# Kernel tuning notes

Hardware: AMD Instinct MI355X
Metric: run time of the kernel (lower is better)

## Reference

```python
import jax, jax.numpy as jnp
import numpy as np

N_NODES = 50000
N_EDGES = 800000
IN_C, HID_C, OUT_C = 256, 256, 128


def gcn_conv(x, W, b, row, col, n_nodes):
    """PyG GCNConv: linear transform, symmetric-normalized aggregation, bias.
    row/col already include self-loops. Messages flow row -> col."""
    h = x @ W  # [N, out]
    deg = jax.ops.segment_sum(jnp.ones_like(col, dtype=h.dtype), col, num_segments=n_nodes)
    d_inv_sqrt = jnp.where(deg > 0, jax.lax.rsqrt(jnp.maximum(deg, 1e-12)), 0.0)
    norm = d_inv_sqrt[row] * d_inv_sqrt[col]  # [E]
    msg = h[row] * norm[:, None]              # gather + scale, [E, out]
    out = jax.ops.segment_sum(msg, col, num_segments=n_nodes)  # scatter-add
    return out + b


def setup_inputs() -> dict:
    key = jax.random.key(0)
    k_x, k_e, k_w1, k_w2 = jax.random.split(key, 4)
    x = jax.random.normal(k_x, (N_NODES, IN_C), dtype=jnp.float32)
    edge_index = jax.random.randint(k_e, (2, N_EDGES), 0, N_NODES, dtype=jnp.int64)
    # Glorot-style init for GCN weights, zeros bias (PyG default)
    s1 = float(np.sqrt(6.0 / (IN_C + HID_C)))
    s2 = float(np.sqrt(6.0 / (HID_C + OUT_C)))
    W1 = jax.random.uniform(k_w1, (IN_C, HID_C), dtype=jnp.float32, minval=-s1, maxval=s1)
    b1 = jnp.zeros((HID_C,), dtype=jnp.float32)
    W2 = jax.random.uniform(k_w2, (HID_C, OUT_C), dtype=jnp.float32, minval=-s2, maxval=s2)
    b2 = jnp.zeros((OUT_C,), dtype=jnp.float32)
    return {"x": x, "edge_index": edge_index, "W1": W1, "b1": b1, "W2": W2, "b2": b2}


def reference(x, edge_index, W1, b1, W2, b2):
    n = x.shape[0]
    # add self-loops (PyG GCNConv default add_self_loops=True)
    loops = jnp.arange(n, dtype=edge_index.dtype)
    row = jnp.concatenate([edge_index[0], loops])
    col = jnp.concatenate([edge_index[1], loops])
    h = gcn_conv(x, W1, b1, row, col, n)
    h = jax.nn.relu(h)  # dropout p=0.0 -> identity
    out = gcn_conv(h, W2, b2, row, col, n)
    return out
```

## Files before the change

### kernel.cpp

```cpp
#include <hip/hip_runtime.h>

#define NN 50000
#define NE 800000
#define IN_C 256
#define HID_C 256
#define OUT_C 128

#define NETP (NE + 8 * NN)
#define NBUCK 196
#define CHUNK 4096
#define NPA 196
#define CAP_B 6400

typedef unsigned short u16;
typedef unsigned int u32;
typedef __attribute__((ext_vector_type(8))) short short8;
typedef __attribute__((ext_vector_type(8))) unsigned short ushort8;
typedef __attribute__((ext_vector_type(4))) float f32x4;
typedef __attribute__((ext_vector_type(2))) float f32x2;
typedef __attribute__((ext_vector_type(4))) unsigned u32x4;

#define CPS ((size_t)(NN + 1) * 32)

__device__ __forceinline__ u16 f2b(float f) {
  unsigned int u = __float_as_uint(f);
  return (u16)((u + 0x7FFFu + ((u >> 16) & 1u)) >> 16);
}
__device__ __forceinline__ float b2f(u16 s) {
  return __uint_as_float(((unsigned int)s) << 16);
}


__global__ __launch_bounds__(256) void convw_zero(const float* __restrict__ W1,
                                                  const float* __restrict__ W2,
                                                  u16* __restrict__ W1t,
                                                  u16* __restrict__ W2t,
                                                  int* __restrict__ cnt,
                                                  u16* __restrict__ Hb,
                                                  int nzb) {
  int b = blockIdx.x;
  if (b < 256) {
    int id = b * 256 + threadIdx.x;
    if (id < 256 * 256) {
      int n = id >> 8, k = id & 255;
      W1t[id] = f2b(W1[k * 256 + n]);
    }
    if (id < 128 * 256) {
      int n = id >> 8, k = id & 255;
      W2t[id] = f2b(W2[k * 128 + n]);
    }
  } else if (b < 256 + nzb) {
    int i = (b - 256) * 256 + threadIdx.x;
    if (i < NN) cnt[i] = 1;
  } else {
    int t = threadIdx.x;
    Hb[(size_t)(t >> 5) * CPS + (size_t)NN * 32 + (t & 31)] = 0;
  }
}


__global__ __launch_bounds__(256) void hist_kernel(const int* __restrict__ col,
                                                   int* __restrict__ cnt, int E) {
  int e = blockIdx.x * blockDim.x + threadIdx.x;
  if (e < E) atomicAdd(&cnt[col[e]], 1);
}

__global__ __launch_bounds__(256) void passA_hist(const int* __restrict__ col,
                                                  int* __restrict__ cntmat, int E) {
  __shared__ int hcnt[256];
  const int blk = blockIdx.x;
  const int tid = threadIdx.x;
  hcnt[tid] = 0;
  __syncthreads();
  const int e0 = blk * CHUNK;
#pragma unroll
  for (int j = 0; j < 16; ++j) {
    int e = e0 + j * 256 + tid;
    if (e < E) atomicAdd(&hcnt[col[e] >> 8], 1);
  }
  __syncthreads();
  cntmat[tid * 256 + blk] = hcnt[tid];
}

__global__ __launch_bounds__(256) void passA_scan(const int* __restrict__ cntmat,
                                                  const int* __restrict__ row_off,
                                                  int* __restrict__ gbase,
                                                  int* __restrict__ btot) {
  __shared__ int wsum[4], wpre[4];
  const int b = blockIdx.x;
  const int tid = threadIdx.x;
  int lane = tid & 63, wid = tid >> 6;
  int v = (tid < NPA) ? cntmat[b * 256 + tid] : 0;
  int s = v;
#pragma unroll
  for (int off = 1; off < 64; off <<= 1) {
    int t = __shfl_up(s, off, 64);
    if (lane >= off) s += t;
  }
  if (lane == 63) wsum[wid] = s;
  __syncthreads();
  if (tid == 0) {
    int acc = 0;
#pragma unroll
    for (int w = 0; w < 4; ++w) { wpre[w] = acc; acc += wsum[w]; }
  }
  __syncthreads();
  int bstart = row_off[b << 8];
  gbase[b * 256 + tid] = bstart + wpre[wid] + (s - v);
  if (tid == 255) btot[b] = wpre[3] + s;
}

__global__ __launch_bounds__(256) void scan1_kernel(const int* __restrict__ cnt,
                                                    int* __restrict__ bsum, int n) {
  __shared__ int ws[4];
  int i = blockIdx.x * 256 + threadIdx.x;
  int lane = threadIdx.x & 63, wid = threadIdx.x >> 6;
  int v = (i < n) ? ((cnt[i] + 7) & ~7) : 0;
#pragma unroll
  for (int off = 32; off > 0; off >>= 1) v += __shfl_down(v, off, 64);
  if (lane == 0) ws[wid] = v;
  __syncthreads();
  if (threadIdx.x == 0) bsum[blockIdx.x] = ws[0] + ws[1] + ws[2] + ws[3];
}

__global__ __launch_bounds__(256) void scan2_kernel(const int* __restrict__ bsum,
                                                    int* __restrict__ boff,
                                                    int* __restrict__ row_off,
                                                    int nb, int n) {
  __shared__ int wsum[4], wpre[5];
  int lane = threadIdx.x & 63, wid = threadIdx.x >> 6;
  int v = (threadIdx.x < nb) ? bsum[threadIdx.x] : 0;
  int s = v;
#pragma unroll
  for (int off = 1; off < 64; off <<= 1) {
    int t = __shfl_up(s, off, 64);
    if (lane >= off) s += t;
  }
  if (lane == 63) wsum[wid] = s;
  __syncthreads();
  if (threadIdx.x == 0) {
    int acc = 0;
#pragma unroll
    for (int w = 0; w < 4; ++w) { wpre[w] = acc; acc += wsum[w]; }
    wpre[4] = acc;
  }
  __syncthreads();
  if (threadIdx.x < nb) boff[threadIdx.x] = wpre[wid] + (s - v);
  if (threadIdx.x == 0) row_off[n] = wpre[4];
}

__global__ __launch_bounds__(256) void scan3_kernel(const int* __restrict__ cnt,
                                                    const int* __restrict__ boff,
                                                    int* __restrict__ row_off,
                                                    float* __restrict__ dinv, int n) {
  __shared__ int wsum[4], wpre[4];
  int i = blockIdx.x * 256 + threadIdx.x;
  int lane = threadIdx.x & 63, wid = threadIdx.x >> 6;
  int vr = (i < n) ? cnt[i] : 0;
  int v = (vr + 7) & ~7;
  int s = v;
#pragma unroll
  for (int off = 1; off < 64; off <<= 1) {
    int t = __shfl_up(s, off, 64);
    if (lane >= off) s += t;
  }
  if (lane == 63) wsum[wid] = s;
  __syncthreads();
  if (threadIdx.x == 0) {
    int acc = 0;
#pragma unroll
    for (int w = 0; w < 4; ++w) { wpre[w] = acc; acc += wsum[w]; }
  }
  __syncthreads();
  if (i < n) {
    int off = boff[blockIdx.x] + wpre[wid] + (s - v);
    row_off[i] = off;
    dinv[i] = rsqrtf((float)vr);
  }
}


template <bool A_IS_F32, bool PLANAR_C>
__device__ __forceinline__ void gemm_body(const void* __restrict__ Ap,
                                          const u16* __restrict__ Bt,
                                          const float* __restrict__ dscale,
                                          u16* __restrict__ C, int M, int N,
                                          int bx, int by,
                                          u16 (&Asl)[2][5120], u16 (&Bsl)[2][5120]) {
  const int tid = threadIdx.x;
  const int row0 = by * 128;
  const int col0 = bx * 128;

  f32x4 acc[4][4] = {};

  const int seg = tid & 7;
  const int rb = tid >> 3;
  const int wave = tid >> 6, lane = tid & 63;
  const int wm = wave >> 1, wn = wave & 1;
  const int qr = lane & 15, quad = lane >> 4;

  float4 aF[4];
  ushort4 aU[4];
  ushort4 bR[4];

  auto load_tiles = [&](int k0) {
    if constexpr (A_IS_F32) {
      const float* A = (const float*)Ap;
#pragma unroll
      for (int i = 0; i < 4; ++i) {
        int gr = row0 + rb + i * 32;
        aF[i] = (gr < M) ? *(const float4*)&A[(size_t)gr * 256 + k0 + seg * 4]
                         : make_float4(0.f, 0.f, 0.f, 0.f);
      }
    } else {
      const u16* A = (const u16*)Ap;
#pragma unroll
      for (int i = 0; i < 4; ++i) {
        int gr = row0 + rb + i * 32;
        aU[i] = (gr < M) ? *(const ushort4*)&A[(size_t)gr * 256 + k0 + seg * 4]
                         : make_ushort4(0, 0, 0, 0);
      }
    }
#pragma unroll
    for (int i = 0; i < 4; ++i) {
      int n = rb + i * 32;
      bR[i] = *(const ushort4*)&Bt[(size_t)(col0 + n) * 256 + k0 + seg * 4];
    }
  };

  auto write_lds = [&](int buf) {
#pragma unroll
    for (int i = 0; i < 4; ++i) {
      int r = rb + i * 32;
      ushort4 u;
      if constexpr (A_IS_F32) {
        u.x = f2b(aF[i].x); u.y = f2b(aF[i].y);
        u.z = f2b(aF[i].z); u.w = f2b(aF[i].w);
      } else {
        u = aU[i];
      }
      *(ushort4*)&Asl[buf][r * 40 + seg * 4] = u;
      *(ushort4*)&Bsl[buf][r * 40 + seg * 4] = bR[i];
    }
  };

  load_tiles(0);
  write_lds(0);
  __syncthreads();

#pragma unroll
  for (int it = 0; it < 8; ++it) {
    const int cur = it & 1;
    if (it < 7) load_tiles((it + 1) * 32);

    short8 afr[4], bfr[4];
#pragma unroll
    for (int mt = 0; mt < 4; ++mt)
      afr[mt] = *(const short8*)&Asl[cur][(wm * 64 + mt * 16 + qr) * 40 + quad * 8];
#pragma unroll
    for (int nt = 0; nt < 4; ++nt)
      bfr[nt] = *(const short8*)&Bsl[cur][(wn * 64 + nt * 16 + qr) * 40 + quad * 8];
#pragma unroll
    for (int mt = 0; mt < 4; ++mt)
#pragma unroll
      for (int nt = 0; nt < 4; ++nt)
        acc[mt][nt] = __builtin_amdgcn_mfma_f32_16x16x32_bf16(afr[mt], bfr[nt], acc[mt][nt], 0, 0, 0);

    if (it < 7) {
      write_lds(1 - cur);
      __syncthreads();
    }
  }

#pragma unroll
  for (int mt = 0; mt < 4; ++mt) {
#pragma unroll
    for (int i = 0; i < 4; ++i) {
      int gr = row0 + wm * 64 + mt * 16 + quad * 4 + i;
      if (gr < M) {
        float sc = dscale[gr];
#pragma unroll
        for (int nt = 0; nt < 4; ++nt) {
          int gc = col0 + wn * 64 + nt * 16 + qr;
          u16 val = f2b(acc[mt][nt][i] * sc);
          if constexpr (PLANAR_C)
            C[(size_t)(gc >> 5) * CPS + (size_t)gr * 32 + (gc & 31)] = val;
          else
            C[(size_t)gr * N + gc] = val;
        }
      }
    }
  }
}

template <bool A_IS_F32, bool PLANAR_C>
__global__ __launch_bounds__(256) void gemm_mfma(const void* __restrict__ Ap,
                                                 const u16* __restrict__ Bt,
                                                 const float* __restrict__ dscale,
                                                 u16* __restrict__ C, int M, int N,
                                                 u16* __restrict__ zrow) {
  if (zrow != nullptr && blockIdx.x == 0 && blockIdx.y == 0 && threadIdx.x < 128) {
    int t = threadIdx.x;
    zrow[(size_t)(t >> 5) * CPS + (size_t)NN * 32 + (t & 31)] = 0;
  }
  __shared__ u16 Asl[2][5120];
  __shared__ u16 Bsl[2][5120];
  gemm_body<A_IS_F32, PLANAR_C>(Ap, Bt, dscale, C, M, N, blockIdx.x, blockIdx.y, Asl, Bsl);
}

__global__ __launch_bounds__(256) void gemm1_scatter(const float* __restrict__ x,
                                                     const u16* __restrict__ W1t,
                                                     const float* __restrict__ dinv,
                                                     u16* __restrict__ Hb, int M, int N,
                                                     int ngb,
                                                     const int* __restrict__ row,
                                                     const int* __restrict__ col,
                                                     const int* __restrict__ gbase,
                                                     uint2* __restrict__ stage, int E) {
  __shared__ u16 ABsl[4][5120];
  int b = blockIdx.x;
  if (b < ngb) {
    gemm_body<true, true>(x, W1t, dinv, Hb, M, N, b & 1, b >> 1,
                          *reinterpret_cast<u16(*)[2][5120]>(&ABsl[0]),
                          *reinterpret_cast<u16(*)[2][5120]>(&ABsl[2]));
  } else {
    uint2* pairs = (uint2*)ABsl;
    int* hcnt = (int*)((char*)ABsl + 32768);
    int* hscan = hcnt + 256;
    int* hbase = hscan + 256;
    int* lcur = hbase + 256;

    const int tid = threadIdx.x;
    const int blk = b - ngb;
    const int e0 = blk * CHUNK;

    hcnt[tid] = 0;
    __syncthreads();

    int ecol[16], erow[16];
#pragma unroll
    for (int j = 0; j < 16; ++j) {
      int e = e0 + j * 256 + tid;
      if (e < E) {
        ecol[j] = col[e];
        erow[j] = row[e];
        atomicAdd(&hcnt[ecol[j] >> 8], 1);
      } else {
        ecol[j] = -1;
      }
    }
    __syncthreads();

    hscan[tid] = hcnt[tid];
    __syncthreads();
#pragma unroll
    for (int off = 1; off < 256; off <<= 1) {
      int t = (tid >= off) ? hscan[tid - off] : 0;
      __syncthreads();
      hscan[tid] += t;
      __syncthreads();
    }

    lcur[tid] = 0;
    hbase[tid] = gbase[tid * 256 + blk];
    __syncthreads();

#pragma unroll
    for (int j = 0; j < 16; ++j) {
      if (ecol[j] >= 0) {
        int bk = ecol[j] >> 8;
        int p = atomicAdd(&lcur[bk], 1);
        pairs[(hscan[bk] - hcnt[bk]) + p] = make_uint2((unsigned)erow[j], (unsigned)ecol[j]);
      }
    }
    __syncthreads();

    int mtot = hscan[255];
    for (int s = tid; s < mtot; s += 256) {
      uint2 pr = pairs[s];
      int bk = (int)(pr.y >> 8);
      stage[hbase[bk] + (s - (hscan[bk] - hcnt[bk]))] = pr;
    }
  }
}

__global__ __launch_bounds__(256) void csr_sort(const uint2* __restrict__ stage,
                                                const int* __restrict__ row_off,
                                                const int* __restrict__ btot,
                                                u16* __restrict__ csrp) {
  __shared__ int cur[256];
  __shared__ u16 outb[CAP_B];
  const int b = blockIdx.x;
  const int base_node = b << 8;
  const int nnodes = min(256, NN - base_node);
  const int tid = threadIdx.x;
  const int bstart = row_off[base_node];
  const int bend = row_off[min(base_node + 256, NN)];
  const int m = bend - bstart;
  const int mm = min(m, CAP_B);
  for (int i = tid; i < mm; i += 256) outb[i] = (u16)NN;
  for (int i = CAP_B + tid; i < m; i += 256) csrp[bstart + i] = (u16)NN;
  __syncthreads();
  if (tid < nnodes) {
    int c0 = row_off[base_node + tid] - bstart;
    outb[c0] = (u16)(base_node + tid);
    cur[tid] = c0 + 1;
  }
  __syncthreads();
  const int mreal = btot[b];
  for (int i = tid; i < mreal; i += 256) {
    uint2 pr = stage[bstart + i];
    int cl = ((int)pr.y - base_node) & 255;
    int p = atomicAdd(&cur[cl], 1);
    if (p < CAP_B) outb[p] = (u16)pr.x;
    else if (bstart + p < NETP) csrp[bstart + p] = (u16)pr.x;
  }
  __syncthreads();
  for (int i = tid; i < mm; i += 256) csrp[bstart + i] = outb[i];
}

template <int NPL, int OUTC, bool RELU_BF16>
__global__ __launch_bounds__(256) void agg_gather(const u16* __restrict__ h,
                                                  const int* __restrict__ row_off,
                                                  const u16* __restrict__ csrp,
                                                  const float* __restrict__ dinv,
                                                  const float* __restrict__ bias,
                                                  void* __restrict__ outp) {
  const int slice = blockIdx.x % NPL;
  const int wave = threadIdx.x >> 6;
  const int lane = threadIdx.x & 63;
  const int nd = lane >> 4;
  const int wg = (lane >> 2) & 3;
  const int c = lane & 3;
  const int v = (blockIdx.x / NPL) * 16 + wave * 4 + nd;
  if (v >= NN) return;
  const u16* hpl = h + (size_t)slice * CPS;
  const int beg = row_off[v], end = row_off[v + 1];
  const int nw = (end - beg) >> 3;
  const int coff = c * 8;

  f32x2 a0 = {}, a1 = {}, a2 = {}, a3 = {};
  for (int w = wg; w < nw; w += 4) {
    ushort8 cw = *(const ushort8*)&csrp[beg + w * 8];
    u32x4 g0 = *(const u32x4*)&hpl[(size_t)cw[0] * 32 + coff];
    u32x4 g1 = *(const u32x4*)&hpl[(size_t)cw[1] * 32 + coff];
    u32x4 g2 = *(const u32x4*)&hpl[(size_t)cw[2] * 32 + coff];
    u32x4 g3 = *(const u32x4*)&hpl[(size_t)cw[3] * 32 + coff];
    u32x4 g4 = *(const u32x4*)&hpl[(size_t)cw[4] * 32 + coff];
    u32x4 g5 = *(const u32x4*)&hpl[(size_t)cw[5] * 32 + coff];
    u32x4 g6 = *(const u32x4*)&hpl[(size_t)cw[6] * 32 + coff];
    u32x4 g7 = *(const u32x4*)&hpl[(size_t)cw[7] * 32 + coff];
#pragma unroll
    for (int q = 0; q < 4; ++q) {
      f32x2 t;
      f32x2 acc = {};
      t[0] = __uint_as_float(g0[q] << 16); t[1] = __uint_as_float(g0[q] & 0xffff0000u); acc += t;
      t[0] = __uint_as_float(g1[q] << 16); t[1] = __uint_as_float(g1[q] & 0xffff0000u); acc += t;
      t[0] = __uint_as_float(g2[q] << 16); t[1] = __uint_as_float(g2[q] & 0xffff0000u); acc += t;
      t[0] = __uint_as_float(g3[q] << 16); t[1] = __uint_as_float(g3[q] & 0xffff0000u); acc += t;
      t[0] = __uint_as_float(g4[q] << 16); t[1] = __uint_as_float(g4[q] & 0xffff0000u); acc += t;
      t[0] = __uint_as_float(g5[q] << 16); t[1] = __uint_as_float(g5[q] & 0xffff0000u); acc += t;
      t[0] = __uint_as_float(g6[q] << 16); t[1] = __uint_as_float(g6[q] & 0xffff0000u); acc += t;
      t[0] = __uint_as_float(g7[q] << 16); t[1] = __uint_as_float(g7[q] & 0xffff0000u); acc += t;
      if (q == 0) a0 += acc;
      else if (q == 1) a1 += acc;
      else if (q == 2) a2 += acc;
      else a3 += acc;
    }
  }
  float aa[8] = {a0[0], a0[1], a1[0], a1[1], a2[0], a2[1], a3[0], a3[1]};
#pragma unroll
  for (int i = 0; i < 8; ++i) {
    aa[i] += __shfl_xor(aa[i], 4, 64);
    aa[i] += __shfl_xor(aa[i], 8, 64);
  }
  if (wg == 0) {
    const int cg = slice * 32 + coff;
    float dv = dinv[v];
    float4 bv0 = *(const float4*)&bias[cg];
    float4 bv1 = *(const float4*)&bias[cg + 4];
    float bb[8] = {bv0.x, bv0.y, bv0.z, bv0.w, bv1.x, bv1.y, bv1.z, bv1.w};
    if constexpr (RELU_BF16) {
      u16* o = (u16*)outp;
      ushort8 ov;
#pragma unroll
      for (int i = 0; i < 8; ++i) ov[i] = (short)f2b(fmaxf(aa[i] * dv + bb[i], 0.f));
      *(ushort8*)&o[(size_t)v * OUTC + cg] = ov;
    } else {
      float* o = (float*)outp;
      float ov[8];
#pragma unroll
      for (int i = 0; i < 8; ++i) ov[i] = aa[i] * dv + bb[i];
      *(float4*)&o[(size_t)v * OUTC + cg] = make_float4(ov[0], ov[1], ov[2], ov[3]);
      *(float4*)&o[(size_t)v * OUTC + cg + 4] = make_float4(ov[4], ov[5], ov[6], ov[7]);
    }
  }
}


extern "C" void kernel_launch(void* const* d_in, const int* in_sizes, int n_in,
                              void* d_out, int out_size, void* d_ws, size_t ws_size,
                              hipStream_t stream) {
  const float* x = (const float*)d_in[0];
  const int* ei = (const int*)d_in[1];
  const float* W1 = (const float*)d_in[2];
  const float* b1 = (const float*)d_in[3];
  const float* W2 = (const float*)d_in[4];
  const float* b2 = (const float*)d_in[5];
  float* out = (float*)d_out;

  const int* row = ei;
  const int* col = ei + NE;

  const int NB = (NN + 255) / 256;

  u16* Hb = (u16*)d_ws;
  u16* H2b = Hb + (size_t)(NN + 1) * 256;
  u16* H3b = H2b + (size_t)NN * 256;
  u16* W1t = H3b + (size_t)(NN + 1) * 128;
  u16* W2t = W1t + 256 * 256;
  int* cnt = (int*)(W2t + 128 * 256);
  int* row_off = cnt + NN;
  float* dinv = (float*)(row_off + NN + 4);
  int* bsum = (int*)(dinv + NN);
  int* boff = bsum + 200;
  int* cntmat = boff + 200;
  int* gbase = cntmat + 256 * 256;
  int* btot = gbase + 256 * 256;
  u16* csrp = (u16*)(btot + 256);
  uint2* stage = (uint2*)H3b;

  convw_zero<<<256 + NB + 1, 256, 0, stream>>>(W1, W2, W1t, W2t, cnt, Hb, NB);
  passA_hist<<<NPA, 256, 0, stream>>>(col, cntmat, NE);
  hist_kernel<<<(NE + 255) / 256, 256, 0, stream>>>(col, cnt, NE);
  scan1_kernel<<<NB, 256, 0, stream>>>(cnt, bsum, NN);
  scan2_kernel<<<1, 256, 0, stream>>>(bsum, boff, row_off, NB, NN);
  scan3_kernel<<<NB, 256, 0, stream>>>(cnt, boff, row_off, dinv, NN);
  passA_scan<<<NBUCK, 256, 0, stream>>>(cntmat, row_off, gbase, btot);

  {
    const int ngb = (HID_C / 128) * ((NN + 127) / 128);
    gemm1_scatter<<<ngb + NPA, 256, 0, stream>>>(x, W1t, dinv, Hb, NN, HID_C, ngb,
                                                 row, col, gbase, stage, NE);
  }
  csr_sort<<<NBUCK, 256, 0, stream>>>(stage, row_off, btot, csrp);

  const int NGB = (NN + 15) / 16;
  agg_gather<8, 256, true><<<NGB * 8, 256, 0, stream>>>(
      Hb, row_off, csrp, dinv, b1, H2b);

  {
    dim3 grid(OUT_C / 128, (NN + 127) / 128);
    gemm_mfma<false, true><<<grid, 256, 0, stream>>>(H2b, W2t, dinv, H3b, NN, OUT_C, H3b);
  }

  agg_gather<4, 128, false><<<NGB * 4, 256, 0, stream>>>(
      H3b, row_off, csrp, dinv, b2, out);
}
```

Baseline: 274.1 us.

## Assign one node per lane quad in gather aggregation, prefetch next CSR chunk

The aggregation kernel now maps 16 nodes per wave (4 lanes per node) instead of 4 nodes per wave with 4 lane groups splitting each node's edge chunks. This drops the cross-lane shuffle reduction and the idle-lane write path. The edge index chunk for the next iteration is loaded one step ahead. Each lane now walks all of a node's edges serially, so load imbalance from degree variance and longer dependency chains per lane may hurt latency hiding. The prefetch also reads one chunk past each node's end.

```diff
diff --git a/kernel.cpp b/kernel.cpp
--- a/kernel.cpp
+++ b/kernel.cpp
@@ -429,27 +429,26 @@
   const int slice = blockIdx.x % NPL;
   const int wave = threadIdx.x >> 6;
   const int lane = threadIdx.x & 63;
-  const int nd = lane >> 4;
-  const int wg = (lane >> 2) & 3;
+  const int nd = lane >> 2;
   const int c = lane & 3;
-  const int v = (blockIdx.x / NPL) * 16 + wave * 4 + nd;
+  const int v = (blockIdx.x / NPL) * 64 + wave * 16 + nd;
   if (v >= NN) return;
   const u16* hpl = h + (size_t)slice * CPS;
   const int beg = row_off[v], end = row_off[v + 1];
-  const int nw = (end - beg) >> 3;
   const int coff = c * 8;
 
   f32x2 a0 = {}, a1 = {}, a2 = {}, a3 = {};
-  for (int w = wg; w < nw; w += 4) {
-    ushort8 cw = *(const ushort8*)&csrp[beg + w * 8];
-    u32x4 g0 = *(const u32x4*)&hpl[(size_t)cw[0] * 32 + coff];
-    u32x4 g1 = *(const u32x4*)&hpl[(size_t)cw[1] * 32 + coff];
-    u32x4 g2 = *(const u32x4*)&hpl[(size_t)cw[2] * 32 + coff];
-    u32x4 g3 = *(const u32x4*)&hpl[(size_t)cw[3] * 32 + coff];
-    u32x4 g4 = *(const u32x4*)&hpl[(size_t)cw[4] * 32 + coff];
-    u32x4 g5 = *(const u32x4*)&hpl[(size_t)cw[5] * 32 + coff];
-    u32x4 g6 = *(const u32x4*)&hpl[(size_t)cw[6] * 32 + coff];
-    u32x4 g7 = *(const u32x4*)&hpl[(size_t)cw[7] * 32 + coff];
+  ushort8 cwA = *(const ushort8*)&csrp[beg];
+  for (int p = beg; p < end; p += 8) {
+    ushort8 cwB = *(const ushort8*)&csrp[p + 8];
+    u32x4 g0 = *(const u32x4*)&hpl[(size_t)cwA[0] * 32 + coff];
+    u32x4 g1 = *(const u32x4*)&hpl[(size_t)cwA[1] * 32 + coff];
+    u32x4 g2 = *(const u32x4*)&hpl[(size_t)cwA[2] * 32 + coff];
+    u32x4 g3 = *(const u32x4*)&hpl[(size_t)cwA[3] * 32 + coff];
+    u32x4 g4 = *(const u32x4*)&hpl[(size_t)cwA[4] * 32 + coff];
+    u32x4 g5 = *(const u32x4*)&hpl[(size_t)cwA[5] * 32 + coff];
+    u32x4 g6 = *(const u32x4*)&hpl[(size_t)cwA[6] * 32 + coff];
+    u32x4 g7 = *(const u32x4*)&hpl[(size_t)cwA[7] * 32 + coff];
 #pragma unroll
     for (int q = 0; q < 4; ++q) {
       f32x2 t;
@@ -467,33 +466,27 @@
       else if (q == 2) a2 += acc;
       else a3 += acc;
     }
+    cwA = cwB;
   }
   float aa[8] = {a0[0], a0[1], a1[0], a1[1], a2[0], a2[1], a3[0], a3[1]};
-#pragma unroll
-  for (int i = 0; i < 8; ++i) {
-    aa[i] += __shfl_xor(aa[i], 4, 64);
-    aa[i] += __shfl_xor(aa[i], 8, 64);
-  }
-  if (wg == 0) {
-    const int cg = slice * 32 + coff;
-    float dv = dinv[v];
-    float4 bv0 = *(const float4*)&bias[cg];
-    float4 bv1 = *(const float4*)&bias[cg + 4];
-    float bb[8] = {bv0.x, bv0.y, bv0.z, bv0.w, bv1.x, bv1.y, bv1.z, bv1.w};
-    if constexpr (RELU_BF16) {
-      u16* o = (u16*)outp;
-      ushort8 ov;
-#pragma unroll
-      for (int i = 0; i < 8; ++i) ov[i] = (short)f2b(fmaxf(aa[i] * dv + bb[i], 0.f));
-      *(ushort8*)&o[(size_t)v * OUTC + cg] = ov;
-    } else {
-      float* o = (float*)outp;
-      float ov[8];
-#pragma unroll
-      for (int i = 0; i < 8; ++i) ov[i] = aa[i] * dv + bb[i];
-      *(float4*)&o[(size_t)v * OUTC + cg] = make_float4(ov[0], ov[1], ov[2], ov[3]);
-      *(float4*)&o[(size_t)v * OUTC + cg + 4] = make_float4(ov[4], ov[5], ov[6], ov[7]);
-    }
+  const int cg = slice * 32 + coff;
+  float dv = dinv[v];
+  float4 bv0 = *(const float4*)&bias[cg];
+  float4 bv1 = *(const float4*)&bias[cg + 4];
+  float bb[8] = {bv0.x, bv0.y, bv0.z, bv0.w, bv1.x, bv1.y, bv1.z, bv1.w};
+  if constexpr (RELU_BF16) {
+    u16* o = (u16*)outp;
+    ushort8 ov;
+#pragma unroll
+    for (int i = 0; i < 8; ++i) ov[i] = (short)f2b(fmaxf(aa[i] * dv + bb[i], 0.f));
+    *(ushort8*)&o[(size_t)v * OUTC + cg] = ov;
+  } else {
+    float* o = (float*)outp;
+    float ov[8];
+#pragma unroll
+    for (int i = 0; i < 8; ++i) ov[i] = aa[i] * dv + bb[i];
+    *(float4*)&o[(size_t)v * OUTC + cg] = make_float4(ov[0], ov[1], ov[2], ov[3]);
+    *(float4*)&o[(size_t)v * OUTC + cg + 4] = make_float4(ov[4], ov[5], ov[6], ov[7]);
   }
 }
 
@@ -545,7 +538,7 @@
   }
   csr_sort<<<NBUCK, 256, 0, stream>>>(stage, row_off, btot, csrp);
 
-  const int NGB = (NN + 15) / 16;
+  const int NGB = (NN + 63) / 64;
   agg_gather<8, 256, true><<<NGB * 8, 256, 0, stream>>>(
       Hb, row_off, csrp, dinv, b1, H2b);
 
```

After: 271.5 us. Within noise of the previous version (-0.9%).
